# Kernel optimization log

Hardware: AMD Instinct MI355X
Metric: run time of the kernel (lower is better)

Reference implementation:

```python
import jax, jax.numpy as jnp
import numpy as np

SEQ_LEN = 4096
EMB = 2048
INP = 457  # totalSyscalls + 1


def setup_inputs() -> dict:
    key = jax.random.key(0)
    ks = jax.random.split(key, 11)
    s_e = 1.0 / np.sqrt(EMB)  # torch LSTM init scale: 1/sqrt(hidden_size)
    s_d = 1.0 / np.sqrt(INP)
    u = lambda k, shape, s: jax.random.uniform(k, shape, jnp.float32, -s, s)
    return {
        "x": jax.random.normal(ks[0], (1, SEQ_LEN, INP), jnp.float32),
        # Encoder LSTM: input_size=INP, hidden_size=EMB
        "enc_Wih": u(ks[1], (4 * EMB, INP), s_e),
        "enc_Whh": u(ks[2], (4 * EMB, EMB), s_e),
        "enc_bih": u(ks[3], (4 * EMB,), s_e),
        "enc_bhh": u(ks[4], (4 * EMB,), s_e),
        # Decoder LSTM: input_size=EMB, hidden_size=INP, proj_size=EMB
        "dec_Wih": u(ks[5], (4 * INP, EMB), s_d),
        "dec_Whh": u(ks[6], (4 * INP, EMB), s_d),
        "dec_bih": u(ks[7], (4 * INP,), s_d),
        "dec_bhh": u(ks[8], (4 * INP,), s_d),
        "dec_Whr": u(ks[9], (EMB, INP), s_d),
    }


def reference(x, enc_Wih, enc_Whh, enc_bih, enc_bhh,
              dec_Wih, dec_Whh, dec_bih, dec_bhh, dec_Whr):
    xs = x.reshape(SEQ_LEN, INP)  # batch dim is structurally 1

    # ---- Encoder: standard LSTM scanned over timesteps (torch gate order i,f,g,o)
    def enc_step(carry, xt):
        h, c = carry
        g = xt @ enc_Wih.T + enc_bih + h @ enc_Whh.T + enc_bhh  # (4*EMB,)
        i, f, gg, o = jnp.split(g, 4)
        c = jax.nn.sigmoid(f) * c + jax.nn.sigmoid(i) * jnp.tanh(gg)
        h = jax.nn.sigmoid(o) * jnp.tanh(c)
        return (h, c), None

    z = jnp.zeros(EMB, x.dtype)
    (h_enc, _), _ = jax.lax.scan(enc_step, (z, z), xs)

    # ---- Decoder: LSTM with projection (hidden_size=INP, proj_size=EMB),
    # feeds its own projected output back in; collects CELL states each step,
    # prepended (torch.cat([cells, out], 0)) => reversed chronological order.
    def dec_step(carry, _):
        xd, h, c = carry
        g = xd @ dec_Wih.T + dec_bih + h @ dec_Whh.T + dec_bhh  # (4*INP,)
        i, f, gg, o = jnp.split(g, 4)
        c = jax.nn.sigmoid(f) * c + jax.nn.sigmoid(i) * jnp.tanh(gg)
        h_raw = jax.nn.sigmoid(o) * jnp.tanh(c)  # (INP,)
        h = h_raw @ dec_Whr.T                     # projected hidden (EMB,)
        return (h, h, c), c

    init = (h_enc, jnp.zeros(EMB, x.dtype), jnp.zeros(INP, x.dtype))
    _, cells = jax.lax.scan(dec_step, init, None, length=SEQ_LEN)  # (SEQ_LEN, INP)
    out = cells[::-1]
    return jax.nn.softmax(out, axis=1)
```

## Files before the change

kernel.cpp:

```cpp
#include <hip/hip_runtime.h>
#include <cmath>

#define SEQ 4096
#define INP 457
#define EMB 2048
#define NWG_E 256
#define NWG_D 16
#define NCPY 8

typedef unsigned long long u64t;
typedef float f32x4 __attribute__((ext_vector_type(4)));
typedef float f32x2 __attribute__((ext_vector_type(2)));

__device__ __forceinline__ float sigf(float v) { return 1.0f / (1.0f + expf(-v)); }

#define PIN(v) asm volatile("" : "+v"(v))
#define QNAN __builtin_bit_cast(float, 0x7fc00000u)

__device__ __forceinline__ f32x4 mall16(const f32x4* p) {
  f32x4 v;
  asm volatile("global_load_dwordx4 %0, %1, off sc0 sc1\n\ts_waitcnt vmcnt(0)"
               : "=v"(v) : "v"(p) : "memory");
  return v;
}
__device__ __forceinline__ f32x2 mall8(const f32x2* p) {
  f32x2 v;
  asm volatile("global_load_dwordx2 %0, %1, off sc0 sc1\n\ts_waitcnt vmcnt(0)"
               : "=v"(v) : "v"(p) : "memory");
  return v;
}

__global__ void bias_kernel(const float* __restrict__ ebih, const float* __restrict__ ebhh,
                            const float* __restrict__ dbih, const float* __restrict__ dbhh,
                            float* __restrict__ bsum, float* __restrict__ btot) {
  int i = blockIdx.x * 256 + threadIdx.x;
  if (i < 4 * EMB) bsum[i] = ebih[i] + ebhh[i];
  if (i < 4 * INP) btot[i] = dbih[i] + dbhh[i];
}

__global__ __launch_bounds__(256) void fold_gemm(const float* __restrict__ dWih,
                                                 const float* __restrict__ dWhh,
                                                 const float* __restrict__ dWhr,
                                                 float* __restrict__ C) {
  const int bx = blockIdx.x, by = blockIdx.y;
  const int tid = threadIdx.x;
  const int tx = tid & 15, ty = tid >> 4;
  __shared__ float As[16][65];
  __shared__ float Bs[16][65];
  float acc[4][4] = {};
  for (int k0 = 0; k0 < EMB; k0 += 16) {
#pragma unroll
    for (int e = 0; e < 4; ++e) {
      int eid = tid * 4 + e;
      int m = eid >> 4, k = eid & 15;
      int row = by * 64 + m;
      float v = 0.0f;
      if (row < 4 * INP) {
        size_t a = (size_t)row * EMB + k0 + k;
        v = dWih[a] + dWhh[a];
      }
      As[k][m] = v;
    }
#pragma unroll
    for (int e = 0; e < 4; ++e) {
      int eid = tid * 4 + e;
      int k = eid >> 6, c = eid & 63;
      int col = bx * 64 + c;
      Bs[k][c] = (col < INP) ? dWhr[(size_t)(k0 + k) * INP + col] : 0.0f;
    }
    __syncthreads();
#pragma unroll
    for (int k = 0; k < 16; ++k) {
      float a0 = As[k][ty * 4 + 0], a1 = As[k][ty * 4 + 1], a2 = As[k][ty * 4 + 2], a3 = As[k][ty * 4 + 3];
      float b0 = Bs[k][tx * 4 + 0], b1 = Bs[k][tx * 4 + 1], b2 = Bs[k][tx * 4 + 2], b3 = Bs[k][tx * 4 + 3];
      acc[0][0] += a0 * b0; acc[0][1] += a0 * b1; acc[0][2] += a0 * b2; acc[0][3] += a0 * b3;
      acc[1][0] += a1 * b0; acc[1][1] += a1 * b1; acc[1][2] += a1 * b2; acc[1][3] += a1 * b3;
      acc[2][0] += a2 * b0; acc[2][1] += a2 * b1; acc[2][2] += a2 * b2; acc[2][3] += a2 * b3;
      acc[3][0] += a3 * b0; acc[3][1] += a3 * b1; acc[3][2] += a3 * b2; acc[3][3] += a3 * b3;
    }
    __syncthreads();
  }
#pragma unroll
  for (int i = 0; i < 4; ++i) {
    int row = by * 64 + ty * 4 + i;
    if (row >= 4 * INP) continue;
#pragma unroll
    for (int j = 0; j < 4; ++j) {
      int col = bx * 64 + tx * 4 + j;
      if (col < 480) C[(size_t)row * 480 + col] = acc[i][j];
    }
  }
}

__global__ __launch_bounds__(512) __attribute__((amdgpu_waves_per_eu(2, 2))) void enc_kernel(
    const float* __restrict__ x, const float* __restrict__ Wih,
    const float* __restrict__ Whh, const float* __restrict__ bsum,
    float* __restrict__ hbuf) {
  const int tid = threadIdx.x;
  const int wg  = blockIdx.x;
  const int j   = tid & 7;
  const int kc  = tid >> 3;
  const int jbase = wg * 8;
  const int mycpy = wg & (NCPY - 1);

  float wh[4][32];
  float wi[4][8];
#pragma unroll
  for (int g = 0; g < 4; ++g) {
    const size_t row = (size_t)(g * EMB + jbase + j);
    const float* wp = Whh + row * EMB + kc * 32;
#pragma unroll
    for (int q = 0; q < 8; ++q) {
      const float4 v = *(const float4*)(wp + 4 * q);
      wh[g][q * 4 + 0] = v.x; wh[g][q * 4 + 1] = v.y;
      wh[g][q * 4 + 2] = v.z; wh[g][q * 4 + 3] = v.w;
    }
    const float* ip = Wih + row * INP;
#pragma unroll
    for (int i = 0; i < 8; ++i) {
      const int c = kc * 8 + i;
      wi[g][i] = (c < INP) ? ip[c] : 0.0f;
    }
  }
#pragma unroll
  for (int g = 0; g < 4; ++g) {
#pragma unroll
    for (int q = 0; q < 32; ++q) PIN(wh[g][q]);
#pragma unroll
    for (int q = 0; q < 8; ++q) PIN(wi[g][q]);
  }

  __shared__ float4 hl4[512];
  __shared__ float4 xl4[128];
  __shared__ float  partbuf[256];
  __shared__ float  b_s[32];
  __shared__ float  c_s[8];
  if (tid < 32) b_s[tid] = bsum[(tid >> 3) * EMB + jbase + (tid & 7)];
  if (tid < 8)  c_s[tid] = 0.0f;
  const int sw = kc & 7;
  const int hphys = tid ^ ((tid >> 3) & 7);
  const int xi = (tid < INP) ? tid : 0;

  for (int t = 0; t < SEQ; ++t) {
    const float xraw = x[(size_t)t * INP + xi];

    const f32x4* gp = (const f32x4*)(hbuf + (size_t)((t & 3) * NCPY + mycpy) * EMB) + tid;
    f32x4 g4;
    for (;;) {
      g4 = mall16(gp);
      if ((g4.x == g4.x) & (g4.y == g4.y) & (g4.z == g4.z) & (g4.w == g4.w)) break;
    }
    hl4[hphys] = make_float4(g4.x, g4.y, g4.z, g4.w);
    ((float*)xl4)[tid] = (tid < INP) ? xraw : 0.0f;

    float4 a0 = make_float4(0, 0, 0, 0), a1 = a0, a2 = a0, a3 = a0;
#pragma unroll
    for (int q = 0; q < 2; ++q) {
      const float4 xq = xl4[kc * 2 + q];
      a0.x += wi[0][q * 4 + 0] * xq.x; a0.y += wi[0][q * 4 + 1] * xq.y; a0.z += wi[0][q * 4 + 2] * xq.z; a0.w += wi[0][q * 4 + 3] * xq.w;
      a1.x += wi[1][q * 4 + 0] * xq.x; a1.y += wi[1][q * 4 + 1] * xq.y; a1.z += wi[1][q * 4 + 2] * xq.z; a1.w += wi[1][q * 4 + 3] * xq.w;
      a2.x += wi[2][q * 4 + 0] * xq.x; a2.y += wi[2][q * 4 + 1] * xq.y; a2.z += wi[2][q * 4 + 2] * xq.z; a2.w += wi[2][q * 4 + 3] * xq.w;
      a3.x += wi[3][q * 4 + 0] * xq.x; a3.y += wi[3][q * 4 + 1] * xq.y; a3.z += wi[3][q * 4 + 2] * xq.z; a3.w += wi[3][q * 4 + 3] * xq.w;
    }
#pragma unroll
    for (int q = 0; q < 8; ++q) {
      const float4 hv = hl4[kc * 8 + (q ^ sw)];
      const int b = q * 4;
      a0.x += wh[0][b + 0] * hv.x; a0.y += wh[0][b + 1] * hv.y; a0.z += wh[0][b + 2] * hv.z; a0.w += wh[0][b + 3] * hv.w;
      a1.x += wh[1][b + 0] * hv.x; a1.y += wh[1][b + 1] * hv.y; a1.z += wh[1][b + 2] * hv.z; a1.w += wh[1][b + 3] * hv.w;
      a2.x += wh[2][b + 0] * hv.x; a2.y += wh[2][b + 1] * hv.y; a2.z += wh[2][b + 2] * hv.z; a2.w += wh[2][b + 3] * hv.w;
      a3.x += wh[3][b + 0] * hv.x; a3.y += wh[3][b + 1] * hv.y; a3.z += wh[3][b + 2] * hv.z; a3.w += wh[3][b + 3] * hv.w;
    }

    float r0 = (a0.x + a0.y) + (a0.z + a0.w);
    float r1 = (a1.x + a1.y) + (a1.z + a1.w);
    float r2 = (a2.x + a2.y) + (a2.z + a2.w);
    float r3 = (a3.x + a3.y) + (a3.z + a3.w);
#pragma unroll
    for (int m = 8; m < 64; m <<= 1) {
      r0 += __shfl_xor(r0, m); r1 += __shfl_xor(r1, m);
      r2 += __shfl_xor(r2, m); r3 += __shfl_xor(r3, m);
    }
    if ((tid & 63) < 8)
      *(float4*)(partbuf + (tid >> 6) * 32 + j * 4) = make_float4(r0, r1, r2, r3);
    __syncthreads();

    if (tid < 8) {
      float s0 = 0.f, s1 = 0.f, s2 = 0.f, s3 = 0.f;
#pragma unroll
      for (int w = 0; w < 8; ++w) {
        const float4 pv = *(const float4*)(partbuf + w * 32 + tid * 4);
        s0 += pv.x; s1 += pv.y; s2 += pv.z; s3 += pv.w;
      }
      const float gi = s0 + b_s[tid], gf = s1 + b_s[8 + tid];
      const float gg = s2 + b_s[16 + tid], go = s3 + b_s[24 + tid];
      const float cN = sigf(gf) * c_s[tid] + sigf(gi) * tanhf(gg);
      c_s[tid] = cN;
      const float hN = sigf(go) * tanhf(cN);
      asm volatile("s_waitcnt vmcnt(0)" ::: "memory");
      float* const pub = hbuf + (size_t)(((t + 1) & 3) * NCPY) * EMB + jbase + tid;
#pragma unroll
      for (int c = 0; c < NCPY; ++c)
        __hip_atomic_store(pub + (size_t)c * EMB, hN,
                           __ATOMIC_RELAXED, __HIP_MEMORY_SCOPE_AGENT);
      float* const rearm = hbuf + (size_t)(((t + 3) & 3) * NCPY) * EMB + jbase + tid;
#pragma unroll
      for (int c = 0; c < NCPY; ++c)
        __hip_atomic_store(rearm + (size_t)c * EMB, QNAN,
                           __ATOMIC_RELAXED, __HIP_MEMORY_SCOPE_AGENT);
    }
  }
}

__global__ __launch_bounds__(512) __attribute__((amdgpu_waves_per_eu(2, 2))) void dec_kernel(
    const float* __restrict__ dWih, const float* __restrict__ Wfold,
    const float* __restrict__ btot, const float* __restrict__ henc,
    float* __restrict__ hraw, float* __restrict__ out) {
  const int tid = threadIdx.x;
  const int wg  = blockIdx.x;
  const int j   = tid & 31;
  const int kc  = tid >> 5;
  const int idx = wg * 32 + j;
  const bool valid = (idx < INP);
  const int id0 = valid ? idx : 0;
  const int l   = tid & 63;
  const int wv  = tid >> 6;
  int gl = l;
  if (gl >= 30) gl -= 30;
  if (gl >= 30) gl -= 30;
  const int gidx = 30 * wv + gl;

  float wd[4][30];
#pragma unroll
  for (int g = 0; g < 4; ++g) {
    const float* wp = Wfold + (size_t)(g * INP + id0) * 480 + kc * 30;
#pragma unroll
    for (int q = 0; q < 15; ++q) {
      const float2 v = valid ? *(const float2*)(wp + 2 * q) : make_float2(0.0f, 0.0f);
      wd[g][q * 2 + 0] = v.x; wd[g][q * 2 + 1] = v.y;
    }
  }
#pragma unroll
  for (int g = 0; g < 4; ++g)
#pragma unroll
    for (int q = 0; q < 30; ++q) PIN(wd[g][q]);

  __shared__ float2 dl2[240];
  __shared__ float  partbuf[1024];
  __shared__ float  b_s[128];
  __shared__ float  c_s[32];
  if (tid < 128) {
    const int ix = wg * 32 + (tid & 31);
    b_s[tid] = (ix < INP) ? btot[(tid >> 5) * INP + ix] : 0.0f;
  }
  if (tid < 32) c_s[tid] = 0.0f;

  for (int t = 0; t < SEQ; ++t) {
    if (t > 0) {
      const f32x2* gp = (const f32x2*)(hraw + (size_t)(t & 3) * 512) + gidx;
      f32x2 g2;
      for (;;) {
        g2 = mall8(gp);
        if ((g2.x == g2.x) & (g2.y == g2.y)) break;
      }
      if (l < 30) dl2[gidx] = make_float2(g2.x, g2.y);
    }

    float2 acc0 = make_float2(0, 0), acc1 = acc0, acc2 = acc0, acc3 = acc0;
    if (t == 0) {
      if (valid) {
#pragma unroll 4
        for (int q = 0; q < 32; ++q) {
          const float4 hv = *(const float4*)(henc + kc * 128 + 4 * q);
          const float4 w0 = *(const float4*)(dWih + (size_t)(0 * INP + idx) * EMB + kc * 128 + 4 * q);
          const float4 w1 = *(const float4*)(dWih + (size_t)(1 * INP + idx) * EMB + kc * 128 + 4 * q);
          const float4 w2 = *(const float4*)(dWih + (size_t)(2 * INP + idx) * EMB + kc * 128 + 4 * q);
          const float4 w3 = *(const float4*)(dWih + (size_t)(3 * INP + idx) * EMB + kc * 128 + 4 * q);
          acc0.x += w0.x * hv.x + w0.z * hv.z; acc0.y += w0.y * hv.y + w0.w * hv.w;
          acc1.x += w1.x * hv.x + w1.z * hv.z; acc1.y += w1.y * hv.y + w1.w * hv.w;
          acc2.x += w2.x * hv.x + w2.z * hv.z; acc2.y += w2.y * hv.y + w2.w * hv.w;
          acc3.x += w3.x * hv.x + w3.z * hv.z; acc3.y += w3.y * hv.y + w3.w * hv.w;
        }
      }
    } else {
#pragma unroll
      for (int q = 0; q < 15; ++q) {
        const float2 hv = dl2[kc * 15 + q];
        acc0.x += wd[0][q * 2] * hv.x; acc0.y += wd[0][q * 2 + 1] * hv.y;
        acc1.x += wd[1][q * 2] * hv.x; acc1.y += wd[1][q * 2 + 1] * hv.y;
        acc2.x += wd[2][q * 2] * hv.x; acc2.y += wd[2][q * 2 + 1] * hv.y;
        acc3.x += wd[3][q * 2] * hv.x; acc3.y += wd[3][q * 2 + 1] * hv.y;
      }
    }
    float r0 = acc0.x + acc0.y, r1 = acc1.x + acc1.y, r2 = acc2.x + acc2.y, r3 = acc3.x + acc3.y;
    r0 += __shfl_xor(r0, 32); r1 += __shfl_xor(r1, 32);
    r2 += __shfl_xor(r2, 32); r3 += __shfl_xor(r3, 32);
    if ((tid & 63) < 32)
      *(float4*)(partbuf + (tid >> 6) * 128 + (tid & 31) * 4) = make_float4(r0, r1, r2, r3);
    __syncthreads();

    if (tid < 32) {
      const int ix = wg * 32 + tid;
      float s0 = 0.f, s1 = 0.f, s2 = 0.f, s3 = 0.f;
#pragma unroll
      for (int w = 0; w < 8; ++w) {
        const float4 pv = *(const float4*)(partbuf + w * 128 + tid * 4);
        s0 += pv.x; s1 += pv.y; s2 += pv.z; s3 += pv.w;
      }
      const float gi = s0 + b_s[tid], gf = s1 + b_s[32 + tid];
      const float gg = s2 + b_s[64 + tid], go = s3 + b_s[96 + tid];
      const float cN = sigf(gf) * c_s[tid] + sigf(gi) * tanhf(gg);
      c_s[tid] = cN;
      const float hrN = sigf(go) * tanhf(cN);
      asm volatile("s_waitcnt vmcnt(0)" ::: "memory");
      if (ix < 480)
        __hip_atomic_store(hraw + (size_t)((t + 1) & 3) * 512 + ix, (ix < INP) ? hrN : 0.0f,
                           __ATOMIC_RELAXED, __HIP_MEMORY_SCOPE_AGENT);
      if (ix < INP) out[(size_t)(SEQ - 1 - t) * INP + ix] = cN;
      if (ix < 480)
        __hip_atomic_store(hraw + (size_t)((t + 3) & 3) * 512 + ix, QNAN,
                           __ATOMIC_RELAXED, __HIP_MEMORY_SCOPE_AGENT);
    }
  }
}

__global__ __launch_bounds__(512) void softmax_kernel(float* __restrict__ out) {
  const int row = blockIdx.x;
  const int tid = threadIdx.x;
  __shared__ float red[512];
  float* rp = out + (size_t)row * INP;
  float v = (tid < INP) ? rp[tid] : -INFINITY;
  red[tid] = v;
  __syncthreads();
#pragma unroll
  for (int off = 256; off > 0; off >>= 1) {
    if (tid < off) red[tid] = fmaxf(red[tid], red[tid + off]);
    __syncthreads();
  }
  const float m = red[0];
  __syncthreads();
  const float e = (tid < INP) ? expf(v - m) : 0.0f;
  red[tid] = e;
  __syncthreads();
#pragma unroll
  for (int off = 256; off > 0; off >>= 1) {
    if (tid < off) red[tid] = red[tid] + red[tid + off];
    __syncthreads();
  }
  const float s = red[0];
  if (tid < INP) rp[tid] = e / s;
}

extern "C" void kernel_launch(void* const* d_in, const int* in_sizes, int n_in,
                              void* d_out, int out_size, void* d_ws, size_t ws_size,
                              hipStream_t stream) {
  const float* x    = (const float*)d_in[0];
  const float* eWih = (const float*)d_in[1];
  const float* eWhh = (const float*)d_in[2];
  const float* ebih = (const float*)d_in[3];
  const float* ebhh = (const float*)d_in[4];
  const float* dWih = (const float*)d_in[5];
  const float* dWhh = (const float*)d_in[6];
  const float* dbih = (const float*)d_in[7];
  const float* dbhh = (const float*)d_in[8];
  const float* dWhr = (const float*)d_in[9];
  float* out = (float*)d_out;
  char* ws = (char*)d_ws;

  float* hbuf  = (float*)(ws + 0);
  float* hraw  = (float*)(ws + 262144);
  float* bsum  = (float*)(ws + 270336);
  float* btot  = (float*)(ws + 303104);
  float* Wfold = (float*)(ws + 311296);

  hipMemsetAsync(ws, 0xFF, 270336, stream);
  hipMemsetAsync(ws, 0x00, 65536, stream);
  bias_kernel<<<40, 256, 0, stream>>>(ebih, ebhh, dbih, dbhh, bsum, btot);
  fold_gemm<<<dim3(8, 29), 256, 0, stream>>>(dWih, dWhh, dWhr, Wfold);
  enc_kernel<<<NWG_E, 512, 0, stream>>>(x, eWih, eWhh, bsum, hbuf);
  dec_kernel<<<NWG_D, 512, 0, stream>>>(dWih, Wfold, btot, hbuf, hraw, out);
  softmax_kernel<<<SEQ, 512, 0, stream>>>(out);
}
```

Baseline: 17.56 ms.

## Replicate decoder hidden-state broadcast buffers and use fast gate activations

The decoder now publishes each step's raw hidden state into four replicated buffers, and each workgroup polls its own copy, mirroring the encoder's scheme. The intent is to spread polling traffic across more cache lines and lower cross-workgroup handoff latency. Sigmoid and tanh now use fast exp and reciprocal intrinsics, and biases and the cell state live in registers instead of shared memory, shortening the serial per-step gate tail. The cost is extra atomic stores per step, a larger workspace layout, and slightly lower activation accuracy.

```diff
diff --git a/kernel.cpp b/kernel.cpp
--- a/kernel.cpp
+++ b/kernel.cpp
@@ -7,12 +7,18 @@
 #define NWG_E 256
 #define NWG_D 16
 #define NCPY 8
+#define NDCPY 4
 
 typedef unsigned long long u64t;
 typedef float f32x4 __attribute__((ext_vector_type(4)));
 typedef float f32x2 __attribute__((ext_vector_type(2)));
 
-__device__ __forceinline__ float sigf(float v) { return 1.0f / (1.0f + expf(-v)); }
+__device__ __forceinline__ float sigf(float v) {
+  return __builtin_amdgcn_rcpf(1.0f + __expf(-v));
+}
+__device__ __forceinline__ float tanhf_fast(float v) {
+  return 1.0f - 2.0f * __builtin_amdgcn_rcpf(__expf(2.0f * v) + 1.0f);
+}
 
 #define PIN(v) asm volatile("" : "+v"(v))
 #define QNAN __builtin_bit_cast(float, 0x7fc00000u)
@@ -129,14 +135,15 @@
 #pragma unroll
     for (int q = 0; q < 8; ++q) PIN(wi[g][q]);
   }
+  const float bg0 = bsum[0 * EMB + jbase + j];
+  const float bg1 = bsum[1 * EMB + jbase + j];
+  const float bg2 = bsum[2 * EMB + jbase + j];
+  const float bg3 = bsum[3 * EMB + jbase + j];
+  float c_reg = 0.0f;
 
   __shared__ float4 hl4[512];
   __shared__ float4 xl4[128];
   __shared__ float  partbuf[256];
-  __shared__ float  b_s[32];
-  __shared__ float  c_s[8];
-  if (tid < 32) b_s[tid] = bsum[(tid >> 3) * EMB + jbase + (tid & 7)];
-  if (tid < 8)  c_s[tid] = 0.0f;
   const int sw = kc & 7;
   const int hphys = tid ^ ((tid >> 3) & 7);
   const int xi = (tid < INP) ? tid : 0;
@@ -192,11 +199,10 @@
         const float4 pv = *(const float4*)(partbuf + w * 32 + tid * 4);
         s0 += pv.x; s1 += pv.y; s2 += pv.z; s3 += pv.w;
       }
-      const float gi = s0 + b_s[tid], gf = s1 + b_s[8 + tid];
-      const float gg = s2 + b_s[16 + tid], go = s3 + b_s[24 + tid];
-      const float cN = sigf(gf) * c_s[tid] + sigf(gi) * tanhf(gg);
-      c_s[tid] = cN;
-      const float hN = sigf(go) * tanhf(cN);
+      const float gi = s0 + bg0, gf = s1 + bg1, gg = s2 + bg2, go = s3 + bg3;
+      const float cN = sigf(gf) * c_reg + sigf(gi) * tanhf_fast(gg);
+      c_reg = cN;
+      const float hN = sigf(go) * tanhf_fast(cN);
       asm volatile("s_waitcnt vmcnt(0)" ::: "memory");
       float* const pub = hbuf + (size_t)(((t + 1) & 3) * NCPY) * EMB + jbase + tid;
 #pragma unroll
@@ -225,6 +231,7 @@
   const int id0 = valid ? idx : 0;
   const int l   = tid & 63;
   const int wv  = tid >> 6;
+  const int mycpy = wg & (NDCPY - 1);
   int gl = l;
   if (gl >= 30) gl -= 30;
   if (gl >= 30) gl -= 30;
@@ -245,19 +252,18 @@
 #pragma unroll
     for (int q = 0; q < 30; ++q) PIN(wd[g][q]);
 
+  const float bg0 = valid ? btot[0 * INP + idx] : 0.0f;
+  const float bg1 = valid ? btot[1 * INP + idx] : 0.0f;
+  const float bg2 = valid ? btot[2 * INP + idx] : 0.0f;
+  const float bg3 = valid ? btot[3 * INP + idx] : 0.0f;
+  float c_reg = 0.0f;
+
   __shared__ float2 dl2[240];
   __shared__ float  partbuf[1024];
-  __shared__ float  b_s[128];
-  __shared__ float  c_s[32];
-  if (tid < 128) {
-    const int ix = wg * 32 + (tid & 31);
-    b_s[tid] = (ix < INP) ? btot[(tid >> 5) * INP + ix] : 0.0f;
-  }
-  if (tid < 32) c_s[tid] = 0.0f;
 
   for (int t = 0; t < SEQ; ++t) {
     if (t > 0) {
-      const f32x2* gp = (const f32x2*)(hraw + (size_t)(t & 3) * 512) + gidx;
+      const f32x2* gp = (const f32x2*)(hraw + (size_t)((t & 3) * NDCPY + mycpy) * 512) + gidx;
       f32x2 g2;
       for (;;) {
         g2 = mall8(gp);
@@ -307,19 +313,25 @@
         const float4 pv = *(const float4*)(partbuf + w * 128 + tid * 4);
         s0 += pv.x; s1 += pv.y; s2 += pv.z; s3 += pv.w;
       }
-      const float gi = s0 + b_s[tid], gf = s1 + b_s[32 + tid];
-      const float gg = s2 + b_s[64 + tid], go = s3 + b_s[96 + tid];
-      const float cN = sigf(gf) * c_s[tid] + sigf(gi) * tanhf(gg);
-      c_s[tid] = cN;
-      const float hrN = sigf(go) * tanhf(cN);
+      const float gi = s0 + bg0, gf = s1 + bg1, gg = s2 + bg2, go = s3 + bg3;
+      const float cN = sigf(gf) * c_reg + sigf(gi) * tanhf_fast(gg);
+      c_reg = cN;
+      const float hrN = sigf(go) * tanhf_fast(cN);
       asm volatile("s_waitcnt vmcnt(0)" ::: "memory");
-      if (ix < 480)
-        __hip_atomic_store(hraw + (size_t)((t + 1) & 3) * 512 + ix, (ix < INP) ? hrN : 0.0f,
-                           __ATOMIC_RELAXED, __HIP_MEMORY_SCOPE_AGENT);
+      if (ix < 480) {
+        const float pv = (ix < INP) ? hrN : 0.0f;
+#pragma unroll
+        for (int c = 0; c < NDCPY; ++c)
+          __hip_atomic_store(hraw + (size_t)(((t + 1) & 3) * NDCPY + c) * 512 + ix, pv,
+                             __ATOMIC_RELAXED, __HIP_MEMORY_SCOPE_AGENT);
+      }
       if (ix < INP) out[(size_t)(SEQ - 1 - t) * INP + ix] = cN;
-      if (ix < 480)
-        __hip_atomic_store(hraw + (size_t)((t + 3) & 3) * 512 + ix, QNAN,
-                           __ATOMIC_RELAXED, __HIP_MEMORY_SCOPE_AGENT);
+      if (ix < 480) {
+#pragma unroll
+        for (int c = 0; c < NDCPY; ++c)
+          __hip_atomic_store(hraw + (size_t)(((t + 3) & 3) * NDCPY + c) * 512 + ix, QNAN,
+                             __ATOMIC_RELAXED, __HIP_MEMORY_SCOPE_AGENT);
+      }
     }
   }
 }
@@ -369,11 +381,11 @@
 
   float* hbuf  = (float*)(ws + 0);
   float* hraw  = (float*)(ws + 262144);
-  float* bsum  = (float*)(ws + 270336);
-  float* btot  = (float*)(ws + 303104);
-  float* Wfold = (float*)(ws + 311296);
-
-  hipMemsetAsync(ws, 0xFF, 270336, stream);
+  float* bsum  = (float*)(ws + 294912);
+  float* btot  = (float*)(ws + 327680);
+  float* Wfold = (float*)(ws + 335872);
+
+  hipMemsetAsync(ws, 0xFF, 294912, stream);
   hipMemsetAsync(ws, 0x00, 65536, stream);
   bias_kernel<<<40, 256, 0, stream>>>(ebih, ebhh, dbih, dbhh, bsum, btot);
   fold_gemm<<<dim3(8, 29), 256, 0, stream>>>(dWih, dWhh, dWhr, Wfold);
```

Result: faster. 15.68 ms (-10.7%).
